# Optimization experiments

Measured on AMD Instinct MI355X. Metric: run time of the kernel, lower is better.

Reference implementation:

```python
import jax, jax.numpy as jnp
import numpy as np

B = 512   # batch (== window_size, required by the original detrend loop)
W = 512   # window_size
E = 512   # emb_dim
EPS = 1e-5


def setup_inputs() -> dict:
    key = jax.random.key(0)
    k = jax.random.split(key, 5)
    x = jax.random.normal(k[0], (B, W, E), dtype=jnp.float32)
    # per-channel Linear(window_size, 1): stacked as [E, W] weights, [E] bias
    W1 = jax.random.normal(k[1], (E, W), dtype=jnp.float32) / np.sqrt(W)
    b1 = jax.random.normal(k[2], (E,), dtype=jnp.float32) * 0.01
    gamma = jnp.ones((E,), dtype=jnp.float32)   # BatchNorm1d(1) weight per channel
    beta = jnp.zeros((E,), dtype=jnp.float32)   # BatchNorm1d(1) bias per channel
    W2 = jax.random.normal(k[3], (E, 1), dtype=jnp.float32) / np.sqrt(E)
    b2 = jnp.zeros((1,), dtype=jnp.float32)
    return {"x": x, "W1": W1, "b1": b1, "gamma": gamma, "beta": beta, "W2": W2, "b2": b2}


def reference(x, W1, b1, gamma, beta, W2, b2):
    # seq_last is detached in the original (no grad through this path)
    seq_last = jax.lax.stop_gradient(x[:, -1, :])          # [B, E]
    xd = x - seq_last[:, None, :]                          # detrend all timesteps
    # E independent Linear(W -> 1), vectorized as one contraction
    lin = jnp.einsum('bwe,ew->be', xd, W1) + b1            # [B, E]
    # BatchNorm1d(1) per channel, training mode: biased var over batch
    mean = jnp.mean(lin, axis=0)                           # [E]
    var = jnp.mean((lin - mean) ** 2, axis=0)              # [E], biased
    bn = (lin - mean) * jax.lax.rsqrt(var + EPS) * gamma + beta
    out = bn + seq_last                                    # [B, E]
    return out @ W2 + b2                                   # [B, 1]
```

## Files before the change

kernel.cpp:

```cpp
#include <hip/hip_runtime.h>
#include <math.h>

#define Bn 512
#define Wn 512
#define En 512
#define EPSF 1e-5f

typedef float fx4 __attribute__((ext_vector_type(4)));

#define O_W1T    0
#define O_LIN    (O_W1T + En * Wn)
#define O_PSUM   (O_LIN + Bn * En)
#define O_PSUMSQ (O_PSUM + 8 * En)

__global__ void k_transpose(const float* __restrict__ w1, float* __restrict__ w1t) {
    __shared__ float tile[32][33];
    int bx = blockIdx.x, by = blockIdx.y;
    int tx = threadIdx.x, ty = threadIdx.y;
#pragma unroll
    for (int j = 0; j < 32; j += 8)
        tile[ty + j][tx] = w1[(size_t)(by * 32 + ty + j) * Wn + bx * 32 + tx];
    __syncthreads();
#pragma unroll
    for (int j = 0; j < 32; j += 8)
        w1t[(size_t)(bx * 32 + ty + j) * En + by * 32 + tx] = tile[tx][ty + j];
}

__global__ __launch_bounds__(512) void k_main(const float* __restrict__ x,
                                              const float* __restrict__ w1t,
                                              const float* __restrict__ b1,
                                              float* __restrict__ lin) {
    int b = blockIdx.x;
    int tid = threadIdx.x;
    int wsub = tid >> 7;
    int e4 = tid & 127;

    const fx4* xp = (const fx4*)x + ((size_t)b * Wn + (size_t)wsub * 128) * (En / 4) + e4;
    const fx4* wp = (const fx4*)w1t + (size_t)(wsub * 128) * (En / 4) + e4;

    fx4 acc = {0.f, 0.f, 0.f, 0.f};
    fx4 wsum = {0.f, 0.f, 0.f, 0.f};
#pragma unroll 8
    for (int w = 0; w < 128; ++w) {
        fx4 xv = __builtin_nontemporal_load(&xp[(size_t)w * (En / 4)]);
        fx4 wv = wp[(size_t)w * (En / 4)];
        acc += xv * wv;
        wsum += wv;
    }

    __shared__ fx4 lacc[4][128];
    __shared__ fx4 lws[4][128];
    lacc[wsub][e4] = acc;
    lws[wsub][e4] = wsum;
    __syncthreads();

    if (wsub == 0) {
        fx4 t = lacc[0][e4], u = lws[0][e4];
#pragma unroll
        for (int k = 1; k < 4; ++k) {
            t += lacc[k][e4];
            u += lws[k][e4];
        }
        fx4 xl = ((const fx4*)x)[((size_t)b * Wn + (Wn - 1)) * (En / 4) + e4];
        fx4 bb = ((const fx4*)b1)[e4];
        fx4 r = t - xl * u + bb;
        ((fx4*)lin)[(size_t)b * (En / 4) + e4] = r;
    }
}

__global__ void k_stats_partial(const float* __restrict__ lin,
                                float* __restrict__ psum, float* __restrict__ psumsq) {
    int blk = blockIdx.x;
    int e = threadIdx.x;
    float s = 0.f, q = 0.f;
    int b0 = blk * 64;
#pragma unroll 4
    for (int b = b0; b < b0 + 64; ++b) {
        float v = lin[(size_t)b * En + e];
        s += v;
        q += v * v;
    }
    psum[blk * En + e] = s;
    psumsq[blk * En + e] = q;
}

__global__ __launch_bounds__(128) void k_out(const float* __restrict__ lin,
                                             const float* __restrict__ x,
                                             const float* __restrict__ psum,
                                             const float* __restrict__ psumsq,
                                             const float* __restrict__ gamma,
                                             const float* __restrict__ beta,
                                             const float* __restrict__ w2,
                                             const float* __restrict__ b2,
                                             float* __restrict__ out) {
    int b = blockIdx.x;
    int t = threadIdx.x;

    fx4 s4 = {0.f, 0.f, 0.f, 0.f}, q4 = {0.f, 0.f, 0.f, 0.f};
#pragma unroll
    for (int c = 0; c < 8; ++c) {
        s4 += ((const fx4*)psum)[c * (En / 4) + t];
        q4 += ((const fx4*)psumsq)[c * (En / 4) + t];
    }
    fx4 g = ((const fx4*)gamma)[t];
    fx4 be = ((const fx4*)beta)[t];
    fx4 mean = s4 * (1.f / Bn);
    fx4 var = q4 * (1.f / Bn) - mean * mean;
    fx4 sc, sh;
    sc.x = g.x * rsqrtf(var.x + EPSF); sc.y = g.y * rsqrtf(var.y + EPSF);
    sc.z = g.z * rsqrtf(var.z + EPSF); sc.w = g.w * rsqrtf(var.w + EPSF);
    sh = be - mean * sc;

    fx4 l  = ((const fx4*)lin)[(size_t)b * (En / 4) + t];
    fx4 xl = ((const fx4*)x)[((size_t)b * Wn + (Wn - 1)) * (En / 4) + t];
    fx4 wv = ((const fx4*)w2)[t];
    fx4 term = (l * sc + sh + xl) * wv;
    float v = term.x + term.y + term.z + term.w;
#pragma unroll
    for (int off = 32; off; off >>= 1) v += __shfl_down(v, off);
    __shared__ float red[2];
    int wid = t >> 6, lane = t & 63;
    if (lane == 0) red[wid] = v;
    __syncthreads();
    if (t == 0) out[b] = red[0] + red[1] + b2[0];
}

extern "C" void kernel_launch(void* const* d_in, const int* in_sizes, int n_in,
                              void* d_out, int out_size, void* d_ws, size_t ws_size,
                              hipStream_t stream) {
    const float* x     = (const float*)d_in[0];
    const float* w1    = (const float*)d_in[1];
    const float* b1    = (const float*)d_in[2];
    const float* gamma = (const float*)d_in[3];
    const float* beta  = (const float*)d_in[4];
    const float* w2    = (const float*)d_in[5];
    const float* b2    = (const float*)d_in[6];
    float* out = (float*)d_out;
    float* ws  = (float*)d_ws;

    float* w1t    = ws + O_W1T;
    float* lin    = ws + O_LIN;
    float* psum   = ws + O_PSUM;
    float* psumsq = ws + O_PSUMSQ;

    k_transpose<<<dim3(Wn / 32, En / 32), dim3(32, 8), 0, stream>>>(w1, w1t);
    k_main<<<Bn, 512, 0, stream>>>(x, w1t, b1, lin);
    k_stats_partial<<<8, 512, 0, stream>>>(lin, psum, psumsq);
    k_out<<<Bn, 128, 0, stream>>>(lin, x, psum, psumsq, gamma, beta, w2, b2, out);
}
```

Before: 108.1 us.

## Fuse BatchNorm statistics into main kernel via last-block atomic counter

Drops the separate stats kernel. Each main-kernel block increments a global atomic counter, and the last block to finish reduces all lin rows into per-channel scale and shift. The output kernel then reads these precomputed values instead of summing partials. This saves one launch, but the final reduction over 512 rows runs serially in a single block on the critical path.

```diff
diff --git a/kernel.cpp b/kernel.cpp
--- a/kernel.cpp
+++ b/kernel.cpp
@@ -10,10 +10,14 @@
 
 #define O_W1T    0
 #define O_LIN    (O_W1T + En * Wn)
-#define O_PSUM   (O_LIN + Bn * En)
-#define O_PSUMSQ (O_PSUM + 8 * En)
+#define O_SCALE  (O_LIN + Bn * En)
+#define O_SHIFT  (O_SCALE + En)
+#define O_CTR    (O_SHIFT + En)
 
-__global__ void k_transpose(const float* __restrict__ w1, float* __restrict__ w1t) {
+__global__ void k_transpose(const float* __restrict__ w1, float* __restrict__ w1t,
+                            unsigned int* __restrict__ ctr) {
+    if (blockIdx.x == 0 && blockIdx.y == 0 && threadIdx.x == 0 && threadIdx.y == 0)
+        *ctr = 0u;
     __shared__ float tile[32][33];
     int bx = blockIdx.x, by = blockIdx.y;
     int tx = threadIdx.x, ty = threadIdx.y;
@@ -29,11 +33,18 @@
 __global__ __launch_bounds__(512) void k_main(const float* __restrict__ x,
                                               const float* __restrict__ w1t,
                                               const float* __restrict__ b1,
-                                              float* __restrict__ lin) {
+                                              const float* __restrict__ gamma,
+                                              const float* __restrict__ beta,
+                                              float* __restrict__ lin,
+                                              float* __restrict__ scale,
+                                              float* __restrict__ shift,
+                                              unsigned int* __restrict__ ctr) {
     int b = blockIdx.x;
     int tid = threadIdx.x;
     int wsub = tid >> 7;
     int e4 = tid & 127;
+
+    fx4 xl = ((const fx4*)x)[((size_t)b * Wn + (Wn - 1)) * (En / 4) + e4];
 
     const fx4* xp = (const fx4*)x + ((size_t)b * Wn + (size_t)wsub * 128) * (En / 4) + e4;
     const fx4* wp = (const fx4*)w1t + (size_t)(wsub * 128) * (En / 4) + e4;
@@ -61,56 +72,49 @@
             t += lacc[k][e4];
             u += lws[k][e4];
         }
-        fx4 xl = ((const fx4*)x)[((size_t)b * Wn + (Wn - 1)) * (En / 4) + e4];
         fx4 bb = ((const fx4*)b1)[e4];
         fx4 r = t - xl * u + bb;
         ((fx4*)lin)[(size_t)b * (En / 4) + e4] = r;
     }
-}
 
-__global__ void k_stats_partial(const float* __restrict__ lin,
-                                float* __restrict__ psum, float* __restrict__ psumsq) {
-    int blk = blockIdx.x;
-    int e = threadIdx.x;
-    float s = 0.f, q = 0.f;
-    int b0 = blk * 64;
-#pragma unroll 4
-    for (int b = b0; b < b0 + 64; ++b) {
-        float v = lin[(size_t)b * En + e];
-        s += v;
-        q += v * v;
+    __shared__ int is_last;
+    __syncthreads();
+    if (tid == 0) {
+        __threadfence();
+        unsigned int old = atomicAdd(ctr, 1u);
+        is_last = (old == Bn - 1u) ? 1 : 0;
     }
-    psum[blk * En + e] = s;
-    psumsq[blk * En + e] = q;
+    __syncthreads();
+    if (is_last) {
+        __threadfence();
+        int e = tid;
+        float s = 0.f, q = 0.f;
+#pragma unroll 8
+        for (int bb2 = 0; bb2 < Bn; ++bb2) {
+            float v = lin[(size_t)bb2 * En + e];
+            s += v;
+            q += v * v;
+        }
+        float mean = s * (1.f / Bn);
+        float var = q * (1.f / Bn) - mean * mean;
+        float sc = gamma[e] * rsqrtf(var + EPSF);
+        scale[e] = sc;
+        shift[e] = beta[e] - mean * sc;
+    }
 }
 
 __global__ __launch_bounds__(128) void k_out(const float* __restrict__ lin,
                                              const float* __restrict__ x,
-                                             const float* __restrict__ psum,
-                                             const float* __restrict__ psumsq,
-                                             const float* __restrict__ gamma,
-                                             const float* __restrict__ beta,
+                                             const float* __restrict__ scale,
+                                             const float* __restrict__ shift,
                                              const float* __restrict__ w2,
                                              const float* __restrict__ b2,
                                              float* __restrict__ out) {
     int b = blockIdx.x;
     int t = threadIdx.x;
 
-    fx4 s4 = {0.f, 0.f, 0.f, 0.f}, q4 = {0.f, 0.f, 0.f, 0.f};
-#pragma unroll
-    for (int c = 0; c < 8; ++c) {
-        s4 += ((const fx4*)psum)[c * (En / 4) + t];
-        q4 += ((const fx4*)psumsq)[c * (En / 4) + t];
-    }
-    fx4 g = ((const fx4*)gamma)[t];
-    fx4 be = ((const fx4*)beta)[t];
-    fx4 mean = s4 * (1.f / Bn);
-    fx4 var = q4 * (1.f / Bn) - mean * mean;
-    fx4 sc, sh;
-    sc.x = g.x * rsqrtf(var.x + EPSF); sc.y = g.y * rsqrtf(var.y + EPSF);
-    sc.z = g.z * rsqrtf(var.z + EPSF); sc.w = g.w * rsqrtf(var.w + EPSF);
-    sh = be - mean * sc;
-
+    fx4 sc = ((const fx4*)scale)[t];
+    fx4 sh = ((const fx4*)shift)[t];
     fx4 l  = ((const fx4*)lin)[(size_t)b * (En / 4) + t];
     fx4 xl = ((const fx4*)x)[((size_t)b * Wn + (Wn - 1)) * (En / 4) + t];
     fx4 wv = ((const fx4*)w2)[t];
@@ -138,13 +142,13 @@
     float* out = (float*)d_out;
     float* ws  = (float*)d_ws;
 
-    float* w1t    = ws + O_W1T;
-    float* lin    = ws + O_LIN;
-    float* psum   = ws + O_PSUM;
-    float* psumsq = ws + O_PSUMSQ;
+    float* w1t   = ws + O_W1T;
+    float* lin   = ws + O_LIN;
+    float* scale = ws + O_SCALE;
+    float* shift = ws + O_SHIFT;
+    unsigned int* ctr = (unsigned int*)(ws + O_CTR);
 
-    k_transpose<<<dim3(Wn / 32, En / 32), dim3(32, 8), 0, stream>>>(w1, w1t);
-    k_main<<<Bn, 512, 0, stream>>>(x, w1t, b1, lin);
-    k_stats_partial<<<8, 512, 0, stream>>>(lin, psum, psumsq);
-    k_out<<<Bn, 128, 0, stream>>>(lin, x, psum, psumsq, gamma, beta, w2, b2, out);
+    k_transpose<<<dim3(Wn / 32, En / 32), dim3(32, 8), 0, stream>>>(w1, w1t, ctr);
+    k_main<<<Bn, 512, 0, stream>>>(x, w1t, b1, gamma, beta, lin, scale, shift, ctr);
+    k_out<<<Bn, 128, 0, stream>>>(lin, x, scale, shift, w2, b2, out);
 }
```

New measurement: 151.3 us. 1.4x slower.
